# Kernel tuning notes

Measured on AMD Instinct MI355X. Metric: run time of the kernel, lower is better.

Reference implementation:

```python
import jax, jax.numpy as jnp
import numpy as np

POOLING_COUNTS = [15, 8, 8]
N = 128
D = 256
B = 16


def _build_specs():
    # Replicates the (kernel, stride, i, j) schedule of SparseConv.__init__.
    specs = []
    stride, offset = 1, 0
    for ci, c in enumerate(POOLING_COUNTS):
        for k in range(c):
            offset += stride
            i = np.arange(0, N - offset, stride)
            j = np.arange(offset, N, stride)
            kern = 3 if (ci > 0 and k == 0) else 2  # first conv of later groups downsamples
            st = 2 if (ci > 0 and k == 0) else 1
            specs.append((kern, st, i, j))
        stride *= 2
    return specs

SPECS = _build_specs()
N_K2 = sum(1 for s in SPECS if s[0] == 2)  # 29 kernel-2 stride-1 convs
N_K3 = sum(1 for s in SPECS if s[0] == 3)  # 2 kernel-3 stride-2 convs


def _conv1d(x, w, b, stride):
    # x: (B, D, L), w: (O, I, K) -> (B, O, L_out), VALID padding like nn.Conv1d
    y = jax.lax.conv_general_dilated(x, w, (stride,), 'VALID',
                                     dimension_numbers=('NCH', 'OIH', 'NCH'))
    return y + b[None, :, None]


def setup_inputs() -> dict:
    key = jax.random.key(0)
    ks = jax.random.split(key, 5)
    scale = 1.0 / np.sqrt(2.0 * D)  # ~ PyTorch Conv1d default init scale
    return {
        'x': jax.random.normal(ks[0], (B, D, N), jnp.float32),
        'w2': jax.random.normal(ks[1], (N_K2, D, D, 2), jnp.float32) * scale,
        'b2': jax.random.normal(ks[2], (N_K2, D), jnp.float32) * scale,
        'w3': jax.random.normal(ks[3], (N_K3, D, D, 3), jnp.float32) * scale,
        'b3': jax.random.normal(ks[4], (N_K3, D), jnp.float32) * scale,
    }


def reference(x, w2, b2, w3, b3):
    diag = np.arange(N)
    # map2d[:, :, i, i] = x
    map2d = jnp.zeros((B, D, N, N), x.dtype).at[:, :, diag, diag].set(x)
    c2 = c3 = 0
    for kern, st, i, j in SPECS:  # fixed-length chain of 31 structurally distinct convs
        if kern == 2:
            x = _conv1d(x, w2[c2], b2[c2], 1)
            c2 += 1
        else:
            x = _conv1d(x, w3[c3], b3[c3], 2)
            c3 += 1
        map2d = map2d.at[:, :, i, j].set(x)  # scatter stripe into sparse 2D map
    return map2d
```

## Files before the change

kernel.cpp:

```cpp
#include <hip/hip_runtime.h>

typedef __bf16 bf16x8 __attribute__((ext_vector_type(8)));
typedef float  floatx4 __attribute__((ext_vector_type(4)));
typedef float  fvec4  __attribute__((ext_vector_type(4)));
typedef unsigned short ushort4v __attribute__((ext_vector_type(4)));
typedef unsigned short ushort8v __attribute__((ext_vector_type(8)));

__device__ __forceinline__ unsigned short f2bf(float f) {
  unsigned int u = __float_as_uint(f);
  u = u + 0x7FFFu + ((u >> 16) & 1u);
  return (unsigned short)(u >> 16);
}

#define WP3_OFF   3801088
#define X0_OFF    4194304
#define TBL_E     16777216
#define Y_OFF_B   (64u << 20)

__global__ __launch_bounds__(256) void prep_kernel(
    const float* __restrict__ w2, const float* __restrict__ w3,
    const float* __restrict__ x, unsigned short* __restrict__ ws)
{
  int g = blockIdx.x * 256 + threadIdx.x;
  const float* src; unsigned short* dst;
  if (g < 950272)            { src = w2; dst = ws; }
  else if (g < 950272+98304) { g -= 950272; src = w3; dst = ws + WP3_OFF; }
  else                       { g -= (950272+98304); src = x; dst = ws + X0_OFF; }
  fvec4 v = *reinterpret_cast<const fvec4*>(src + 4*g);
  ushort4v o;
  o[0] = f2bf(v[0]); o[1] = f2bf(v[1]); o[2] = f2bf(v[2]); o[3] = f2bf(v[3]);
  *reinterpret_cast<ushort4v*>(dst + 4*g) = o;
}

__global__ __launch_bounds__(256) void tbl_kernel(unsigned short* __restrict__ tbl)
{
  const int g = blockIdx.x * 256 + threadIdx.x;
  const int h = g >> 13, rl = (g >> 7) & 63, c = g & 127;
  const int r = h * 64 + rl, d = c - r;
  unsigned short v = 0xFFFFu;
  if (d == 0) v = (unsigned short)(31 * 65 + rl);
  else if (d >= 1 && d <= 15) v = (unsigned short)((d - 1) * 65 + rl);
  else if (d >= 17 && d <= 31 && (d & 1) == 1 && (r & 1) == 0)
    v = (unsigned short)((15 + ((d - 17) >> 1)) * 65 + (rl >> 1));
  else if (d >= 35 && d <= 63 && (d & 3) == 3 && (r & 3) == 0)
    v = (unsigned short)((23 + ((d - 35) >> 2)) * 65 + (rl >> 2));
  tbl[g] = v;
}

template<int KW>
__global__ __launch_bounds__(256) void conv_kernel(
    const unsigned short* __restrict__ Xin,
    unsigned short* __restrict__ Xout,
    const unsigned short* __restrict__ WP,
    const float* __restrict__ bias,
    float* __restrict__ Yl,
    int Lpin, int Lout, int Lpout)
{
  constexpr int CS    = (KW == 3) ? 2 : 1;
  constexpr int KS    = 256 * KW;
  constexpr int pitch = KS + 8;
  constexpr int SPAN  = CS * 15 + KW;
  constexpr int NV    = (SPAN + 7) / 8;
  __shared__ unsigned short LA[16 * pitch];

  const int tid = threadIdx.x;
  const int b   = blockIdx.z;
  const int m0  = blockIdx.x * 16;
  const int n0  = blockIdx.y * 64;

  {
    const int i = tid;
    const unsigned short* rp = Xin + ((b * 256 + i) * Lpin) + CS * m0;
    ushort8v xr[NV];
#pragma unroll
    for (int v = 0; v < NV; ++v)
      xr[v] = *reinterpret_cast<const ushort8v*>(rp + v * 8);
    const unsigned short* xs = reinterpret_cast<const unsigned short*>(xr);
    if (KW == 2) {
#pragma unroll
      for (int m = 0; m < 16; ++m) {
        unsigned int pk = (unsigned int)xs[m] | ((unsigned int)xs[m + 1] << 16);
        *reinterpret_cast<unsigned int*>(&LA[m * pitch + 2 * i]) = pk;
      }
    } else {
#pragma unroll
      for (int m = 0; m < 16; ++m) {
        int base = m * pitch + 3 * i;
        LA[base]     = xs[2 * m];
        LA[base + 1] = xs[2 * m + 1];
        LA[base + 2] = xs[2 * m + 2];
      }
    }
  }
  __syncthreads();

  const int wave = tid >> 6, lane = tid & 63;
  const int l15 = lane & 15, quad = lane >> 4;
  const int nn = n0 + wave * 16 + l15;
  const float bv = bias[nn];
  const unsigned short* wrow = WP + (long)nn * KS + quad * 8;

  floatx4 acc = {0.f, 0.f, 0.f, 0.f};
  constexpr int niter = KS / 32;
#pragma unroll
  for (int kc = 0; kc < niter; ++kc) {
    bf16x8 bfrag = *reinterpret_cast<const bf16x8*>(wrow + kc * 32);
    bf16x8 a = *reinterpret_cast<const bf16x8*>(&LA[l15 * pitch + quad * 8 + kc * 32]);
    acc = __builtin_amdgcn_mfma_f32_16x16x32_bf16(a, bfrag, acc, 0, 0, 0);
  }

  const int row = b * 256 + nn;
  unsigned short* xo = Xout + (long)row * Lpout;
  float* yo = Yl + (long)row * 128;
#pragma unroll
  for (int r = 0; r < 4; ++r) {
    const int m = m0 + quad * 4 + r;
    if (m < Lout) {
      const float v = acc[r] + bv;
      xo[m] = f2bf(v);
      yo[m] = v;
    }
  }
}

__global__ __launch_bounds__(256) void assemble_kernel(
    float* __restrict__ out, const float* __restrict__ x,
    const unsigned short* __restrict__ tbl, const float* __restrict__ Y)
{
  __shared__ float S[32 * 65];
  const int bh = blockIdx.x;
  const int blk = bh >> 1, h = bh & 1;
  const int tid = threadIdx.x;

  ushort4v t4s[8];
  const unsigned short* tb = tbl + h * 8192;
#pragma unroll
  for (int it = 0; it < 8; ++it)
    t4s[it] = *reinterpret_cast<const ushort4v*>(tb + 4 * (it * 256 + tid));

#pragma unroll
  for (int p = 0; p < 8; ++p) {
    const int idx = p * 256 + tid;
    const int slot = idx >> 6, m = idx & 63;
    if (slot < 15) {
      const int mm = h * 64 + m;
      if (mm < 127 - slot) S[slot * 65 + m] = Y[(long)slot * 524288 + blk * 128 + mm];
    } else if (slot < 23) {
      if (m < 32) {
        const int mm = h * 32 + m;
        const int Lout = (slot == 15) ? 56 : (71 - slot);
        if (mm < Lout) S[slot * 65 + m] = Y[(long)slot * 524288 + blk * 128 + mm];
      }
    } else if (slot < 31) {
      if (m < 16) {
        const int mm = h * 16 + m;
        const int Lout = (slot == 23) ? 24 : (47 - slot);
        if (mm < Lout) S[slot * 65 + m] = Y[(long)slot * 524288 + blk * 128 + mm];
      }
    } else {
      S[31 * 65 + m] = x[blk * 128 + h * 64 + m];
    }
  }
  __syncthreads();

  const long obase = ((long)blk << 14) + ((long)h << 13);
#pragma unroll
  for (int it = 0; it < 8; ++it) {
    const int flat = it * 256 + tid;
    const ushort4v t4 = t4s[it];
    fvec4 v;
#pragma unroll
    for (int jj = 0; jj < 4; ++jj) {
      const unsigned short t = t4[jj];
      const int idx = (t == 0xFFFFu) ? 0 : (int)t;
      const float sv = S[idx];
      v[jj] = (t == 0xFFFFu) ? 0.f : sv;
    }
    *reinterpret_cast<fvec4*>(out + obase + 4 * flat) = v;
  }
}

extern "C" void kernel_launch(void* const* d_in, const int* in_sizes, int n_in,
                              void* d_out, int out_size, void* d_ws, size_t ws_size,
                              hipStream_t stream)
{
  const float* x  = (const float*)d_in[0];
  const float* w2 = (const float*)d_in[1];
  const float* b2 = (const float*)d_in[2];
  const float* w3 = (const float*)d_in[3];
  const float* b3 = (const float*)d_in[4];
  float* out = (float*)d_out;
  unsigned short* ws = (unsigned short*)d_ws;
  unsigned short* tbl = ws + TBL_E;
  float* Y = (float*)((char*)d_ws + Y_OFF_B);

  prep_kernel<<<4608, 256, 0, stream>>>(w2, w3, x, ws);
  tbl_kernel<<<64, 256, 0, stream>>>(tbl);

  const int counts[3] = {15, 8, 8};
  int stride = 1, offset = 0;
  int Lin = 128, Lpin = 128;
  int c2 = 0, c3 = 0, lidx = 0;
  long xprev = X0_OFF;
  long xnext = xprev + (long)16 * 256 * 128 + 64;
  for (int ci = 0; ci < 3; ++ci) {
    for (int k = 0; k < counts[ci]; ++k) {
      offset += stride;
      int KW = (ci > 0 && k == 0) ? 3 : 2;
      int cs = (KW == 3) ? 2 : 1;
      int Lout = (Lin - KW) / cs + 1;
      int Lpout = (Lout + 7) & ~7;
      const unsigned short* WPt; const float* bt;
      if (KW == 2) { WPt = ws + (long)c2 * 131072; bt = b2 + c2 * 256; ++c2; }
      else         { WPt = ws + WP3_OFF + (long)c3 * 196608; bt = b3 + c3 * 256; ++c3; }
      dim3 grid((Lout + 15) / 16, 4, 16);
      if (KW == 2)
        conv_kernel<2><<<grid, 256, 0, stream>>>(
            ws + xprev, ws + xnext, WPt, bt, Y + (long)lidx * 524288,
            Lpin, Lout, Lpout);
      else
        conv_kernel<3><<<grid, 256, 0, stream>>>(
            ws + xprev, ws + xnext, WPt, bt, Y + (long)lidx * 524288,
            Lpin, Lout, Lpout);
      ++lidx;
      xprev = xnext;
      xnext += (long)16 * 256 * Lpout + 64;
      Lin = Lout; Lpin = Lpout;
    }
    stride *= 2;
  }

  assemble_kernel<<<8192, 256, 0, stream>>>(out, x, tbl, Y);
}
```

Baseline: 562.3 us.

## Store activations as pre-im2col swizzled rows and load via global_load_lds

Each conv's epilogue now writes its bf16 output directly in the next layer's im2col layout: per position, K-packed rows with an XOR swizzle. The next conv can then fill LDS with direct global-to-LDS 16-byte loads instead of per-thread gather and repacking. Each block also covers 32 output positions with two accumulators, so every weight fragment is reused twice. The cost is duplicated activation storage (2-3x), scattered 2-byte epilogue stores, and a larger LDS footprint per block.

```diff
diff --git a/kernel.cpp b/kernel.cpp
--- a/kernel.cpp
+++ b/kernel.cpp
@@ -4,7 +4,6 @@
 typedef float  floatx4 __attribute__((ext_vector_type(4)));
 typedef float  fvec4  __attribute__((ext_vector_type(4)));
 typedef unsigned short ushort4v __attribute__((ext_vector_type(4)));
-typedef unsigned short ushort8v __attribute__((ext_vector_type(8)));
 
 __device__ __forceinline__ unsigned short f2bf(float f) {
   unsigned int u = __float_as_uint(f);
@@ -12,24 +11,46 @@
   return (unsigned short)(u >> 16);
 }
 
+__device__ __forceinline__ void gload_lds16(const unsigned short* g, unsigned short* l) {
+  __builtin_amdgcn_global_load_lds(
+      (const __attribute__((address_space(1))) unsigned int*)(g),
+      (__attribute__((address_space(3))) unsigned int*)(l), 16, 0, 0);
+}
+
 #define WP3_OFF   3801088
-#define X0_OFF    4194304
-#define TBL_E     16777216
-#define Y_OFF_B   (64u << 20)
+#define XC0_E     8388608
+#define TBL_E     47185920
+#define Y_B       100663296
 
 __global__ __launch_bounds__(256) void prep_kernel(
     const float* __restrict__ w2, const float* __restrict__ w3,
     const float* __restrict__ x, unsigned short* __restrict__ ws)
 {
   int g = blockIdx.x * 256 + threadIdx.x;
-  const float* src; unsigned short* dst;
-  if (g < 950272)            { src = w2; dst = ws; }
-  else if (g < 950272+98304) { g -= 950272; src = w3; dst = ws + WP3_OFF; }
-  else                       { g -= (950272+98304); src = x; dst = ws + X0_OFF; }
-  fvec4 v = *reinterpret_cast<const fvec4*>(src + 4*g);
-  ushort4v o;
-  o[0] = f2bf(v[0]); o[1] = f2bf(v[1]); o[2] = f2bf(v[2]); o[3] = f2bf(v[3]);
-  *reinterpret_cast<ushort4v*>(dst + 4*g) = o;
+  if (g < 1048576) {
+    const float* src; unsigned short* dst;
+    if (g < 950272) { src = w2; dst = ws; }
+    else            { g -= 950272; src = w3; dst = ws + WP3_OFF; }
+    fvec4 v = *reinterpret_cast<const fvec4*>(src + 4 * g);
+    ushort4v o;
+    o[0] = f2bf(v[0]); o[1] = f2bf(v[1]); o[2] = f2bf(v[2]); o[3] = f2bf(v[3]);
+    *reinterpret_cast<ushort4v*>(dst + 4 * g) = o;
+  } else {
+    const int h = g - 1048576;
+    const long f = (long)4 * h;
+    const int bb = (int)(f >> 15);
+    const int i  = (int)((f >> 7) & 255);
+    const int p0 = (int)(f & 127);
+    fvec4 v = *reinterpret_cast<const fvec4*>(x + f);
+    unsigned short* xb = ws + XC0_E + (long)bb * 65536;
+#pragma unroll
+    for (int j = 0; j < 4; ++j) {
+      const int p = p0 + j;
+      const unsigned short bf = f2bf(v[j]);
+      xb[p * 512 + ((2 * i) ^ ((p & 7) << 3))] = bf;
+      if (p >= 1) xb[(p - 1) * 512 + ((2 * i + 1) ^ (((p - 1) & 7) << 3))] = bf;
+    }
+  }
 }
 
 __global__ __launch_bounds__(256) void tbl_kernel(unsigned short* __restrict__ tbl)
@@ -47,78 +68,80 @@
   tbl[g] = v;
 }
 
-template<int KW>
+template<int KW, int KWN>
 __global__ __launch_bounds__(256) void conv_kernel(
     const unsigned short* __restrict__ Xin,
     unsigned short* __restrict__ Xout,
     const unsigned short* __restrict__ WP,
     const float* __restrict__ bias,
     float* __restrict__ Yl,
-    int Lpin, int Lout, int Lpout)
-{
-  constexpr int CS    = (KW == 3) ? 2 : 1;
+    int Lout)
+{
+  constexpr int WROW  = 256 * KW;
+  constexpr int BSTR  = (KW == 2) ? 65536 : 49152;
+  constexpr int BSTRN = (KWN == 3) ? 49152 : 65536;
   constexpr int KS    = 256 * KW;
-  constexpr int pitch = KS + 8;
-  constexpr int SPAN  = CS * 15 + KW;
-  constexpr int NV    = (SPAN + 7) / 8;
-  __shared__ unsigned short LA[16 * pitch];
-
-  const int tid = threadIdx.x;
-  const int b   = blockIdx.z;
-  const int m0  = blockIdx.x * 16;
-  const int n0  = blockIdx.y * 64;
+  constexpr int NLD   = (KW == 2) ? 8 : 12;
+  __shared__ unsigned short LA[32 * WROW];
+
+  const int tid = threadIdx.x, wave = tid >> 6, lane = tid & 63;
+  const int b = blockIdx.z, m0 = blockIdx.x * 32, n0 = blockIdx.y * 64;
 
   {
-    const int i = tid;
-    const unsigned short* rp = Xin + ((b * 256 + i) * Lpin) + CS * m0;
-    ushort8v xr[NV];
-#pragma unroll
-    for (int v = 0; v < NV; ++v)
-      xr[v] = *reinterpret_cast<const ushort8v*>(rp + v * 8);
-    const unsigned short* xs = reinterpret_cast<const unsigned short*>(xr);
-    if (KW == 2) {
-#pragma unroll
-      for (int m = 0; m < 16; ++m) {
-        unsigned int pk = (unsigned int)xs[m] | ((unsigned int)xs[m + 1] << 16);
-        *reinterpret_cast<unsigned int*>(&LA[m * pitch + 2 * i]) = pk;
-      }
-    } else {
-#pragma unroll
-      for (int m = 0; m < 16; ++m) {
-        int base = m * pitch + 3 * i;
-        LA[base]     = xs[2 * m];
-        LA[base + 1] = xs[2 * m + 1];
-        LA[base + 2] = xs[2 * m + 2];
-      }
-    }
+    const unsigned short* src = Xin + (long)b * BSTR + (long)m0 * WROW
+                              + wave * (NLD * 512) + lane * 8;
+    unsigned short* dst = &LA[wave * (NLD * 512)];
+#pragma unroll
+    for (int v = 0; v < NLD; ++v)
+      gload_lds16(src + v * 512, dst + v * 512);
   }
   __syncthreads();
 
-  const int wave = tid >> 6, lane = tid & 63;
   const int l15 = lane & 15, quad = lane >> 4;
   const int nn = n0 + wave * 16 + l15;
   const float bv = bias[nn];
   const unsigned short* wrow = WP + (long)nn * KS + quad * 8;
-
-  floatx4 acc = {0.f, 0.f, 0.f, 0.f};
-  constexpr int niter = KS / 32;
-#pragma unroll
-  for (int kc = 0; kc < niter; ++kc) {
+  const int sx = (l15 & 7) << 3;
+
+  floatx4 acc0 = {0.f, 0.f, 0.f, 0.f};
+  floatx4 acc1 = {0.f, 0.f, 0.f, 0.f};
+#pragma unroll
+  for (int kc = 0; kc < KS / 32; ++kc) {
     bf16x8 bfrag = *reinterpret_cast<const bf16x8*>(wrow + kc * 32);
-    bf16x8 a = *reinterpret_cast<const bf16x8*>(&LA[l15 * pitch + quad * 8 + kc * 32]);
-    acc = __builtin_amdgcn_mfma_f32_16x16x32_bf16(a, bfrag, acc, 0, 0, 0);
+    const int ko = (quad * 8 + kc * 32) ^ sx;
+    bf16x8 a0 = *reinterpret_cast<const bf16x8*>(&LA[l15 * WROW + ko]);
+    bf16x8 a1 = *reinterpret_cast<const bf16x8*>(&LA[(16 + l15) * WROW + ko]);
+    acc0 = __builtin_amdgcn_mfma_f32_16x16x32_bf16(a0, bfrag, acc0, 0, 0, 0);
+    acc1 = __builtin_amdgcn_mfma_f32_16x16x32_bf16(a1, bfrag, acc1, 0, 0, 0);
   }
 
   const int row = b * 256 + nn;
-  unsigned short* xo = Xout + (long)row * Lpout;
   float* yo = Yl + (long)row * 128;
-#pragma unroll
-  for (int r = 0; r < 4; ++r) {
-    const int m = m0 + quad * 4 + r;
-    if (m < Lout) {
-      const float v = acc[r] + bv;
-      xo[m] = f2bf(v);
-      yo[m] = v;
+  unsigned short* xb = (KWN != 0) ? (Xout + (long)b * BSTRN) : (unsigned short*)0;
+#pragma unroll
+  for (int half = 0; half < 2; ++half) {
+    const floatx4& A = half ? acc1 : acc0;
+#pragma unroll
+    for (int r = 0; r < 4; ++r) {
+      const int m = m0 + half * 16 + quad * 4 + r;
+      if (m < Lout) {
+        const float v = A[r] + bv;
+        yo[m] = v;
+        const unsigned short bf = f2bf(v);
+        if constexpr (KWN == 2) {
+          xb[m * 512 + ((2 * nn) ^ ((m & 7) << 3))] = bf;
+          if (m >= 1) xb[(m - 1) * 512 + ((2 * nn + 1) ^ (((m - 1) & 7) << 3))] = bf;
+        } else if constexpr (KWN == 3) {
+          if ((m & 1) == 0) {
+            const int mh = m >> 1;
+            xb[mh * 768 + ((3 * nn) ^ ((mh & 7) << 3))] = bf;
+            if (m >= 2) xb[(mh - 1) * 768 + ((3 * nn + 2) ^ (((mh - 1) & 7) << 3))] = bf;
+          } else {
+            const int mh = m >> 1;
+            xb[mh * 768 + ((3 * nn + 1) ^ ((mh & 7) << 3))] = bf;
+          }
+        }
+      }
     }
   }
 }
@@ -192,42 +215,35 @@
   float* out = (float*)d_out;
   unsigned short* ws = (unsigned short*)d_ws;
   unsigned short* tbl = ws + TBL_E;
-  float* Y = (float*)((char*)d_ws + Y_OFF_B);
+  float* Y = (float*)((char*)d_ws + Y_B);
 
   prep_kernel<<<4608, 256, 0, stream>>>(w2, w3, x, ws);
   tbl_kernel<<<64, 256, 0, stream>>>(tbl);
 
-  const int counts[3] = {15, 8, 8};
-  int stride = 1, offset = 0;
-  int Lin = 128, Lpin = 128;
-  int c2 = 0, c3 = 0, lidx = 0;
-  long xprev = X0_OFF;
-  long xnext = xprev + (long)16 * 256 * 128 + 64;
-  for (int ci = 0; ci < 3; ++ci) {
-    for (int k = 0; k < counts[ci]; ++k) {
-      offset += stride;
-      int KW = (ci > 0 && k == 0) ? 3 : 2;
-      int cs = (KW == 3) ? 2 : 1;
-      int Lout = (Lin - KW) / cs + 1;
-      int Lpout = (Lout + 7) & ~7;
-      const unsigned short* WPt; const float* bt;
-      if (KW == 2) { WPt = ws + (long)c2 * 131072; bt = b2 + c2 * 256; ++c2; }
-      else         { WPt = ws + WP3_OFF + (long)c3 * 196608; bt = b3 + c3 * 256; ++c3; }
-      dim3 grid((Lout + 15) / 16, 4, 16);
-      if (KW == 2)
-        conv_kernel<2><<<grid, 256, 0, stream>>>(
-            ws + xprev, ws + xnext, WPt, bt, Y + (long)lidx * 524288,
-            Lpin, Lout, Lpout);
-      else
-        conv_kernel<3><<<grid, 256, 0, stream>>>(
-            ws + xprev, ws + xnext, WPt, bt, Y + (long)lidx * 524288,
-            Lpin, Lout, Lpout);
-      ++lidx;
-      xprev = xnext;
-      xnext += (long)16 * 256 * Lpout + 64;
-      Lin = Lout; Lpin = Lpout;
-    }
-    stride *= 2;
+  long cin = XC0_E;
+  int Lin = 128;
+  int c2 = 0, c3 = 0;
+  for (int l = 0; l < 31; ++l) {
+    const int KW = (l == 15 || l == 23) ? 3 : 2;
+    const int cs = (KW == 3) ? 2 : 1;
+    const int Lout = (Lin - KW) / cs + 1;
+    const int KWN = (l == 30) ? 0 : ((l == 14 || l == 22) ? 3 : 2);
+    const long cnext = cin + (long)16 * ((KW == 2) ? 65536 : 49152);
+    const unsigned short* WPt; const float* bt;
+    if (KW == 2) { WPt = ws + (long)c2 * 131072; bt = b2 + c2 * 256; ++c2; }
+    else         { WPt = ws + WP3_OFF + (long)c3 * 196608; bt = b3 + c3 * 256; ++c3; }
+    dim3 grid((Lout + 31) / 32, 4, 16);
+    float* Yl = Y + (long)l * 524288;
+    if (KW == 2 && KWN == 2)
+      conv_kernel<2,2><<<grid, 256, 0, stream>>>(ws + cin, ws + cnext, WPt, bt, Yl, Lout);
+    else if (KW == 2 && KWN == 3)
+      conv_kernel<2,3><<<grid, 256, 0, stream>>>(ws + cin, ws + cnext, WPt, bt, Yl, Lout);
+    else if (KW == 3 && KWN == 2)
+      conv_kernel<3,2><<<grid, 256, 0, stream>>>(ws + cin, ws + cnext, WPt, bt, Yl, Lout);
+    else
+      conv_kernel<2,0><<<grid, 256, 0, stream>>>(ws + cin, (unsigned short*)0, WPt, bt, Yl, Lout);
+    cin = cnext;
+    Lin = Lout;
   }
 
   assemble_kernel<<<8192, 256, 0, stream>>>(out, x, tbl, Y);
```

New measurement: 523.7 us. 1.07x faster.
